# Performance work log

Measured on AMD Instinct MI355X. Metric: run time of the kernel, lower is better.

The kernel has to match this reference:

```python
import jax, jax.numpy as jnp
import numpy as np

N_NODES = 100000
NEG_SLOPE = 0.2  # PyG GATConv default negative_slope


def gat_layer(x, src, dst, W, a_src, a_dst, b):
    """PyG-style GATConv (eval mode: dropout = identity), concat=True.
    x: [N, F_in]; W: [F_in, H*C]; a_src/a_dst: [H, C]; b: [H*C].
    src/dst: [E] edge endpoints (messages flow src -> dst), self-loops included.
    """
    N = x.shape[0]
    H, C = a_src.shape
    h = (x @ W).reshape(N, H, C)                       # [N, H, C]
    al_s = jnp.sum(h * a_src, axis=-1)                 # [N, H]
    al_d = jnp.sum(h * a_dst, axis=-1)                 # [N, H]
    e = jax.nn.leaky_relu(al_s[src] + al_d[dst], NEG_SLOPE)  # [E, H]
    # softmax over incoming edges of each dst node (every node has a self-loop)
    m = jax.ops.segment_max(e, dst, num_segments=N)    # [N, H]
    ex = jnp.exp(e - m[dst])
    s = jax.ops.segment_sum(ex, dst, num_segments=N)   # [N, H]
    alpha = ex / s[dst]                                # [E, H]
    out = jax.ops.segment_sum(h[src] * alpha[:, :, None], dst, num_segments=N)
    return out.reshape(N, H * C) + b


def setup_inputs() -> dict:
    key = jax.random.key(0)
    ks = jax.random.split(key, 12)
    F_in, Hc, H, n_cls = 128, 32, 4, 3
    x = jax.random.normal(ks[0], (N_NODES, F_in), dtype=jnp.float32)
    edge_index = jax.random.randint(ks[1], (2, 1600000), 0, N_NODES, dtype=jnp.int64)
    sc1 = 1.0 / np.sqrt(F_in)
    sc2 = 1.0 / np.sqrt(Hc * H)
    return {
        "x": x,
        "edge_index": edge_index,
        "W1": jax.random.normal(ks[2], (F_in, H * Hc), dtype=jnp.float32) * sc1,
        "a1_src": jax.random.normal(ks[3], (H, Hc), dtype=jnp.float32) * sc1,
        "a1_dst": jax.random.normal(ks[4], (H, Hc), dtype=jnp.float32) * sc1,
        "b1": jnp.zeros((H * Hc,), dtype=jnp.float32),
        "W2": jax.random.normal(ks[5], (H * Hc, Hc), dtype=jnp.float32) * sc2,
        "a2_src": jax.random.normal(ks[6], (1, Hc), dtype=jnp.float32) * sc2,
        "a2_dst": jax.random.normal(ks[7], (1, Hc), dtype=jnp.float32) * sc2,
        "b2": jnp.zeros((Hc,), dtype=jnp.float32),
        "lin_W": jax.random.normal(ks[8], (Hc, n_cls), dtype=jnp.float32) * (1.0 / np.sqrt(Hc)),
        "lin_b": jnp.zeros((n_cls,), dtype=jnp.float32),
    }


def reference(x, edge_index, W1, a1_src, a1_dst, b1, W2, a2_src, a2_dst, b2, lin_W, lin_b):
    N = x.shape[0]
    loops = jnp.arange(N, dtype=edge_index.dtype)
    src = jnp.concatenate([edge_index[0], loops])
    dst = jnp.concatenate([edge_index[1], loops])
    h = jax.nn.elu(gat_layer(x, src, dst, W1, a1_src, a1_dst, b1))
    h = gat_layer(h, src, dst, W2, a2_src, a2_dst, b2)
    pooled = h.mean(axis=0, keepdims=True)             # batch=None path: [1, Hc]
    return jax.nn.softmax(pooled @ lin_W + lin_b, axis=1)
```

## Files before the change

### kernel.cpp

```cpp
#include <hip/hip_runtime.h>
#include <cstdint>
#include <cstddef>

static inline size_t align_up(size_t v, size_t a) { return (v + a - 1) & ~(a - 1); }

#define BCAP 3072

typedef __attribute__((ext_vector_type(8))) short short8;
typedef __attribute__((ext_vector_type(4))) float f32x4;
typedef __attribute__((ext_vector_type(2))) float f32x2;

__device__ inline unsigned short bf16_1(float x) {
  unsigned u = __float_as_uint(x);
  u += 0x7FFFu + ((u >> 16) & 1u);
  return (unsigned short)(u >> 16);
}
__device__ inline unsigned bfpack(float x, float y) {
  unsigned ux = __float_as_uint(x); ux += 0x7FFFu + ((ux >> 16) & 1u);
  unsigned uy = __float_as_uint(y); uy += 0x7FFFu + ((uy >> 16) & 1u);
  return (ux >> 16) | (uy & 0xFFFF0000u);
}

__device__ inline unsigned char fp8_1(float x) {
  return (unsigned char)(__builtin_amdgcn_cvt_pk_fp8_f32(x, x, 0, false) & 0xFF);
}
__device__ inline f32x2 fp8x2_dec(unsigned us) {
  return __builtin_amdgcn_cvt_pk_f32_fp8((int)us, false);
}

__global__ void detect_kernel(const unsigned int* e, int n_check, int* flag) {
  __shared__ int bad;
  if (threadIdx.x == 0) bad = 0;
  __syncthreads();
  for (int i = threadIdx.x; i < n_check; i += blockDim.x)
    if (e[2 * i + 1] != 0u) bad = 1;
  __syncthreads();
  if (threadIdx.x == 0) *flag = bad ? 0 : 1;
}

__device__ inline int load_edge(const void* eidx, int is64, size_t idx) {
  if (is64) return (int)((const long long*)eidx)[idx];
  return ((const int*)eidx)[idx];
}

__global__ void prep_kernel(const float* __restrict__ W1, const float* __restrict__ W2,
                            unsigned short* __restrict__ w1t, unsigned short* __restrict__ w2t) {
  int t = blockIdx.x * 256 + threadIdx.x;
  if (t < 16384) {
    int c = t >> 7, k = t & 127;
    w1t[t] = bf16_1(W1[(size_t)k * 128 + c]);
  } else if (t < 20480) {
    int i = t - 16384;
    int c = i >> 7, k = i & 127;
    w2t[i] = bf16_1(W2[(size_t)k * 32 + c]);
  }
}


__global__ __launch_bounds__(256) void sortA_kernel(const void* eidx, const int* flag, int E,
                                                    int* __restrict__ fillB,
                                                    unsigned* __restrict__ packed, int NB) {
  __shared__ int hist[1024];
  __shared__ int loff[1024];
  __shared__ int lbase[1024];
  __shared__ int lcnt[1024];
  __shared__ unsigned sortedV[2048];
  __shared__ unsigned short sortedB[2048];
  const int t = threadIdx.x;
  const int chunk0 = blockIdx.x * 2048;
  const int cntE = min(2048, E - chunk0);
  const int is64 = *flag;
  int sv[8], dv[8];
  for (int i = t; i < 1024; i += 256) { hist[i] = 0; lcnt[i] = 0; }
  __syncthreads();
#pragma unroll
  for (int it = 0; it < 8; ++it) {
    int li = it * 256 + t;
    if (li < cntE) {
      sv[it] = load_edge(eidx, is64, (size_t)chunk0 + li);
      dv[it] = load_edge(eidx, is64, (size_t)E + chunk0 + li);
      atomicAdd(&hist[dv[it] >> 7], 1);
    }
  }
  __syncthreads();
  for (int b = t; b < NB; b += 256) {
    int h = hist[b];
    if (h) lbase[b] = b * BCAP + atomicAdd(&fillB[b], h);
  }
  {
    int base = t * 4;
    int v[4]; int s = 0;
    __shared__ int sd[256];
#pragma unroll
    for (int j = 0; j < 4; ++j) { v[j] = hist[base + j]; s += v[j]; }
    sd[t] = s; __syncthreads();
    for (int off = 1; off < 256; off <<= 1) {
      int u = (t >= off) ? sd[t - off] : 0;
      __syncthreads();
      sd[t] += u;
      __syncthreads();
    }
    int run = sd[t] - s;
#pragma unroll
    for (int j = 0; j < 4; ++j) { loff[base + j] = run; run += v[j]; }
  }
  __syncthreads();
#pragma unroll
  for (int it = 0; it < 8; ++it) {
    int li = it * 256 + t;
    if (li < cntE) {
      int b = dv[it] >> 7;
      int r = atomicAdd(&lcnt[b], 1);
      int pos = loff[b] + r;
      sortedV[pos] = (unsigned)sv[it] | ((unsigned)(dv[it] & 127) << 20);
      sortedB[pos] = (unsigned short)b;
    }
  }
  __syncthreads();
  for (int li = t; li < cntE; li += 256) {
    int b = sortedB[li];
    packed[(size_t)lbase[b] + (li - loff[b])] = sortedV[li];
  }
}

__global__ __launch_bounds__(256) void buildCSR_kernel(const unsigned* __restrict__ packed,
                                                       const int* __restrict__ fillB,
                                                       int* __restrict__ rowbeg,
                                                       int* __restrict__ rowend,
                                                       int* __restrict__ csr, int N, int NB) {
  __shared__ int cnt[128], ex[128], fill[128];
  const int b = blockIdx.x;
  const int t = threadIdx.x;
  const int beg = b * BCAP;
  const int end = beg + fillB[b];
  const int node0 = b << 7;
  const int nn = min(128, N - node0);
  if (t < 128) { cnt[t] = 0; fill[t] = 0; }
  __syncthreads();
  for (int i = beg + t; i < end; i += 256) {
    int j = (packed[i] >> 20) & 127;
    atomicAdd(&cnt[j], 1);
  }
  __syncthreads();
  if (t < 128) ex[t] = cnt[t];
  __syncthreads();
  for (int off = 1; off < 128; off <<= 1) {
    int u = (t >= off && t < 128) ? ex[t - off] : 0;
    __syncthreads();
    if (t < 128) ex[t] += u;
    __syncthreads();
  }
  if (t < 128) ex[t] -= cnt[t];
  __syncthreads();
  if (t < nn) {
    rowbeg[node0 + t] = beg + ex[t];
    rowend[node0 + t] = beg + ex[t] + cnt[t];
  }
  for (int i = beg + t; i < end; i += 256) {
    unsigned v = packed[i];
    int j = (v >> 20) & 127;
    int r = atomicAdd(&fill[j], 1);
    csr[beg + ex[j] + r] = (int)(v & 0xFFFFFu);
  }
}

__global__ __launch_bounds__(256) void gemm1_mfma(
    const float* __restrict__ x, const unsigned short* __restrict__ w1t,
    const float* __restrict__ a1s, const float* __restrict__ a1d,
    unsigned char* __restrict__ h1f, float* __restrict__ al1s, float* __restrict__ al1d, int N) {
  __shared__ unsigned short sw[128 * 136];
  __shared__ unsigned short sx[64 * 136];
  unsigned char* ftile = (unsigned char*)sx;
  const int t = threadIdx.x;
  const int row0 = blockIdx.x * 64;
  for (int i = t; i < 4096; i += 256) {
    int c = i >> 5, k4 = (i & 31) * 4;
    *(ushort4*)&sw[c * 136 + k4] = *(const ushort4*)&w1t[c * 128 + k4];
  }
  for (int i = t; i < 2048; i += 256) {
    int r = i >> 5, c4 = (i & 31) * 4;
    float4 v = make_float4(0.f, 0.f, 0.f, 0.f);
    if (row0 + r < N) v = *(const float4*)(x + (size_t)(row0 + r) * 128 + c4);
    ushort4 b; b.x = bf16_1(v.x); b.y = bf16_1(v.y); b.z = bf16_1(v.z); b.w = bf16_1(v.w);
    *(ushort4*)&sx[r * 136 + c4] = b;
  }
  __syncthreads();
  const int lane = t & 63, wave = t >> 6;
  const int m = lane & 15, quad = lane >> 4;
  const unsigned short* arow = &sx[(wave * 16 + m) * 136];
  short8 A[4];
#pragma unroll
  for (int ks = 0; ks < 4; ++ks) A[ks] = *(const short8*)&arow[ks * 32 + quad * 8];
  __syncthreads();
  const int lrow = wave * 16 + quad * 4;
#pragma unroll
  for (int nt = 0; nt < 8; ++nt) {
    const unsigned short* brow = &sw[(nt * 16 + m) * 136];
    f32x4 acc = {0.f, 0.f, 0.f, 0.f};
#pragma unroll
    for (int ks = 0; ks < 4; ++ks) {
      short8 B = *(const short8*)&brow[ks * 32 + quad * 8];
      acc = __builtin_amdgcn_mfma_f32_16x16x32_bf16(A[ks], B, acc, 0, 0, 0);
    }
#pragma unroll
    for (int r = 0; r < 4; ++r)
      ftile[(lrow + r) * 128 + nt * 16 + m] = fp8_1(acc[r]);
  }
  __syncthreads();
#pragma unroll
  for (int it = 0; it < 2; ++it) {
    int row = it * 32 + (t >> 3);
    int chunk = t & 7;
    uint4 v = *(const uint4*)&ftile[row * 128 + chunk * 16];
    int grow = row0 + row;
    if (grow < N) *(uint4*)&h1f[(size_t)grow * 128 + chunk * 16] = v;
    unsigned w[4] = {v.x, v.y, v.z, v.w};
    float ps = 0.f, pd = 0.f;
    int cb = chunk * 16;
#pragma unroll
    for (int q = 0; q < 4; ++q) {
      f32x2 lo = __builtin_amdgcn_cvt_pk_f32_fp8((int)w[q], false);
      f32x2 hi = __builtin_amdgcn_cvt_pk_f32_fp8((int)w[q], true);
      int c = cb + q * 4;
      ps += lo[0] * a1s[c] + lo[1] * a1s[c + 1] + hi[0] * a1s[c + 2] + hi[1] * a1s[c + 3];
      pd += lo[0] * a1d[c] + lo[1] * a1d[c + 1] + hi[0] * a1d[c + 2] + hi[1] * a1d[c + 3];
    }
    ps += __shfl_xor(ps, 1); pd += __shfl_xor(pd, 1);
    if ((chunk & 1) == 0 && grow < N) {
      int head = chunk >> 1;
      al1s[(size_t)grow * 4 + head] = ps;
      al1d[(size_t)grow * 4 + head] = pd;
    }
  }
}

__global__ __launch_bounds__(256) void gemm2_mfma(
    const unsigned* __restrict__ houtb, const unsigned short* __restrict__ w2t,
    const float* __restrict__ a2s, const float* __restrict__ a2d,
    unsigned char* __restrict__ h2f, float* __restrict__ al2s, float* __restrict__ al2d, int N) {
  __shared__ unsigned short sw[32 * 136];
  __shared__ unsigned short sx[64 * 136];
  unsigned char* ftile = (unsigned char*)sx;
  const int t = threadIdx.x;
  const int row0 = blockIdx.x * 64;
  for (int i = t; i < 1024; i += 256) {
    int c = i >> 5, k4 = (i & 31) * 4;
    *(ushort4*)&sw[c * 136 + k4] = *(const ushort4*)&w2t[c * 128 + k4];
  }
  for (int i = t; i < 2048; i += 256) {
    int r = i >> 5, d2 = (i & 31) * 2;
    uint2 v = make_uint2(0u, 0u);
    if (row0 + r < N) v = *(const uint2*)(houtb + (size_t)(row0 + r) * 64 + d2);
    *(uint2*)&sx[r * 136 + d2 * 2] = v;
  }
  __syncthreads();
  const int lane = t & 63, wave = t >> 6;
  const int m = lane & 15, quad = lane >> 4;
  const unsigned short* arow = &sx[(wave * 16 + m) * 136];
  short8 A[4];
#pragma unroll
  for (int ks = 0; ks < 4; ++ks) A[ks] = *(const short8*)&arow[ks * 32 + quad * 8];
  __syncthreads();
  const int lrow = wave * 16 + quad * 4;
#pragma unroll
  for (int nt = 0; nt < 2; ++nt) {
    const unsigned short* brow = &sw[(nt * 16 + m) * 136];
    f32x4 acc = {0.f, 0.f, 0.f, 0.f};
#pragma unroll
    for (int ks = 0; ks < 4; ++ks) {
      short8 B = *(const short8*)&brow[ks * 32 + quad * 8];
      acc = __builtin_amdgcn_mfma_f32_16x16x32_bf16(A[ks], B, acc, 0, 0, 0);
    }
#pragma unroll
    for (int r = 0; r < 4; ++r)
      ftile[(lrow + r) * 32 + nt * 16 + m] = fp8_1(acc[r]);
  }
  __syncthreads();
  if (t < 128) {
    int row = t >> 1, chunk = t & 1;
    uint4 v = *(const uint4*)&ftile[row * 32 + chunk * 16];
    int grow = row0 + row;
    if (grow < N) *(uint4*)&h2f[(size_t)grow * 32 + chunk * 16] = v;
    unsigned w[4] = {v.x, v.y, v.z, v.w};
    float ps = 0.f, pd = 0.f;
    int cb = chunk * 16;
#pragma unroll
    for (int q = 0; q < 4; ++q) {
      f32x2 lo = __builtin_amdgcn_cvt_pk_f32_fp8((int)w[q], false);
      f32x2 hi = __builtin_amdgcn_cvt_pk_f32_fp8((int)w[q], true);
      int c = cb + q * 4;
      ps += lo[0] * a2s[c] + lo[1] * a2s[c + 1] + hi[0] * a2s[c + 2] + hi[1] * a2s[c + 3];
      pd += lo[0] * a2d[c] + lo[1] * a2d[c + 1] + hi[0] * a2d[c + 2] + hi[1] * a2d[c + 3];
    }
    ps += __shfl_xor(ps, 1); pd += __shfl_xor(pd, 1);
    if (chunk == 0 && grow < N) { al2s[grow] = ps; al2d[grow] = pd; }
  }
}

__global__ __launch_bounds__(256) void agg1_kernel(
    const int* __restrict__ rowbeg, const int* __restrict__ rowend, const int* __restrict__ csr_src,
    const unsigned* __restrict__ h1w,
    const float* __restrict__ al_s, const float* __restrict__ al_d,
    const float* __restrict__ b1, unsigned* __restrict__ houtb, int N) {
  int t = threadIdx.x;
  int d = (blockIdx.x * 256 + t) >> 6;
  if (d >= N) return;
  int lane = t & 63;
  int half = lane >> 5;
  int l32 = lane & 31;
  int headq = l32 >> 3;
  int combo_e = l32 >> 2;
  int combo_h = l32 & 3;
  float ald_c = al_d[(size_t)d * 4 + combo_h];
  float acc0, acc1, acc2, acc3, den;
  {
    float e = al_s[(size_t)d * 4 + headq] + al_d[(size_t)d * 4 + headq];
    e = fmaxf(e, 0.2f * e);
    float ex = half == 0 ? __expf(e) : 0.f;
    unsigned hv = h1w[(size_t)d * 32 + l32];
    f32x2 lo = __builtin_amdgcn_cvt_pk_f32_fp8((int)hv, false);
    f32x2 hi = __builtin_amdgcn_cvt_pk_f32_fp8((int)hv, true);
    acc0 = ex * lo[0]; acc1 = ex * lo[1]; acc2 = ex * hi[0]; acc3 = ex * hi[1];
    den = ex;
  }
  int beg = rowbeg[d], end = rowend[d];
  for (int i = beg; i < end; i += 8) {
    int idx = i + combo_e;
    int sj = (idx < end) ? csr_src[idx] : d;
    float e = al_s[(size_t)sj * 4 + combo_h] + ald_c;
    e = fmaxf(e, 0.2f * e);
    float ex = __expf(e);
    if (idx >= end) ex = 0.f;
#pragma unroll
    for (int j = 0; j < 4; ++j) {
      int my_e = 2 * j + half;
      int s = __shfl(sj, my_e * 4);
      float exj = __shfl(ex, my_e * 4 + headq);
      unsigned hv = h1w[(size_t)s * 32 + l32];
      f32x2 lo = __builtin_amdgcn_cvt_pk_f32_fp8((int)hv, false);
      f32x2 hi = __builtin_amdgcn_cvt_pk_f32_fp8((int)hv, true);
      acc0 += exj * lo[0]; acc1 += exj * lo[1];
      acc2 += exj * hi[0]; acc3 += exj * hi[1];
      den += exj;
    }
  }
  acc0 += __shfl_xor(acc0, 32);
  acc1 += __shfl_xor(acc1, 32);
  acc2 += __shfl_xor(acc2, 32);
  acc3 += __shfl_xor(acc3, 32);
  den  += __shfl_xor(den, 32);
  float inv = 1.f / den;
  float4 bv = *(const float4*)(b1 + 4 * l32);
  float o0 = acc0 * inv + bv.x;
  float o1 = acc1 * inv + bv.y;
  float o2 = acc2 * inv + bv.z;
  float o3 = acc3 * inv + bv.w;
  o0 = o0 > 0.f ? o0 : expm1f(o0);
  o1 = o1 > 0.f ? o1 : expm1f(o1);
  o2 = o2 > 0.f ? o2 : expm1f(o2);
  o3 = o3 > 0.f ? o3 : expm1f(o3);
  if (half == 0) {
    uint2 u; u.x = bfpack(o0, o1); u.y = bfpack(o2, o3);
    *(uint2*)&houtb[(size_t)d * 64 + 2 * l32] = u;
  }
}

__global__ __launch_bounds__(256) void agg2_kernel(
    const int* __restrict__ rowbeg, const int* __restrict__ rowend, const int* __restrict__ csr_src,
    const unsigned short* __restrict__ h2q,
    const float* __restrict__ al_s, const float* __restrict__ al_d,
    float* __restrict__ partial, int N) {
  __shared__ float sp[16 * 32];
  int t = threadIdx.x;
  int lane = t & 63;
  int l16 = t & 15;
  int slot = t >> 4;
  int node = (blockIdx.x * 256 + t) >> 4;
  float ox = 0.f, oy = 0.f;
  if (node < N) {
    float ald = al_d[node];
    float accx, accy, den;
    {
      float e = al_s[node] + ald;
      e = fmaxf(e, 0.2f * e);
      float ex = __expf(e);
      f32x2 h = fp8x2_dec(h2q[(size_t)node * 16 + l16]);
      accx = ex * h[0]; accy = ex * h[1]; den = ex;
    }
    int beg = rowbeg[node], end = rowend[node];
    for (int i = beg; i < end; i += 8) {
      int idx = i + (l16 & 7);
      int sj = (idx < end) ? csr_src[idx] : node;
      float e = al_s[sj] + ald;
      e = fmaxf(e, 0.2f * e);
      float ex = __expf(e);
      if (idx >= end) ex = 0.f;
#pragma unroll
      for (int j = 0; j < 8; ++j) {
        int lsrc = (lane & 48) | j;
        int s = __shfl(sj, lsrc);
        float exj = __shfl(ex, lsrc);
        f32x2 h = fp8x2_dec(h2q[(size_t)s * 16 + l16]);
        accx += exj * h[0];
        accy += exj * h[1];
        den += exj;
      }
    }
    float inv = 1.f / den;
    ox = accx * inv; oy = accy * inv;
  }
  sp[slot * 32 + 2 * l16] = ox;
  sp[slot * 32 + 2 * l16 + 1] = oy;
  __syncthreads();
  if (t < 32) {
    float s = 0.f;
#pragma unroll
    for (int j = 0; j < 16; ++j) s += sp[j * 32 + t];
    partial[(size_t)blockIdx.x * 32 + t] = s;
  }
}

__global__ __launch_bounds__(256) void reduce_kernel(
    const float* __restrict__ partial, int nb, float* __restrict__ partial2) {
  __shared__ float sp[8 * 32];
  int t = threadIdx.x;
  int slot = t >> 5, c = t & 31;
  int row0 = blockIdx.x * 8 + slot;
  float s = 0.f;
  for (int i = row0; i < nb; i += 1024) s += partial[(size_t)i * 32 + c];
  sp[slot * 32 + c] = s;
  __syncthreads();
  if (t < 32) {
    float tot = 0.f;
#pragma unroll
    for (int j = 0; j < 8; ++j) tot += sp[j * 32 + t];
    partial2[(size_t)blockIdx.x * 32 + t] = tot;
  }
}

__global__ void final_kernel(const float* __restrict__ partial2, int nb,
                             const float* __restrict__ b2, const float* __restrict__ linW,
                             const float* __restrict__ linb, float* __restrict__ out, int N) {
  __shared__ float sd[256];
  __shared__ float pooled[32];
  int t = threadIdx.x;
  int c = t & 31, g = t >> 5;
  float s = 0.f;
  for (int i = g; i < nb; i += 8) s += partial2[(size_t)i * 32 + c];
  sd[t] = s; __syncthreads();
  if (t < 32) {
    float tot = 0.f;
#pragma unroll
    for (int j = 0; j < 8; ++j) tot += sd[j * 32 + t];
    pooled[t] = tot / (float)N + b2[t];
  }
  __syncthreads();
  if (t == 0) {
    float lg[3];
    for (int j = 0; j < 3; ++j) lg[j] = linb[j];
    for (int cc = 0; cc < 32; ++cc)
      for (int j = 0; j < 3; ++j) lg[j] += pooled[cc] * linW[cc * 3 + j];
    float m = fmaxf(lg[0], fmaxf(lg[1], lg[2]));
    float e0 = __expf(lg[0] - m), e1 = __expf(lg[1] - m), e2 = __expf(lg[2] - m);
    float inv = 1.f / (e0 + e1 + e2);
    out[0] = e0 * inv; out[1] = e1 * inv; out[2] = e2 * inv;
  }
}

extern "C" void kernel_launch(void* const* d_in, const int* in_sizes, int n_in,
                              void* d_out, int out_size, void* d_ws, size_t ws_size,
                              hipStream_t stream) {
  const float* x    = (const float*)d_in[0];
  const void*  eidx = d_in[1];
  const float* W1   = (const float*)d_in[2];
  const float* a1s  = (const float*)d_in[3];
  const float* a1d  = (const float*)d_in[4];
  const float* b1   = (const float*)d_in[5];
  const float* W2   = (const float*)d_in[6];
  const float* a2s  = (const float*)d_in[7];
  const float* a2d  = (const float*)d_in[8];
  const float* b2   = (const float*)d_in[9];
  const float* linW = (const float*)d_in[10];
  const float* linb = (const float*)d_in[11];
  float* out = (float*)d_out;

  const int N = in_sizes[0] / 128;
  const int E = in_sizes[1] / 2;
  const int NB = (N + 127) >> 7;

  char* ws = (char*)d_ws;
  size_t off = 0;
  auto alloc = [&](size_t bytes) -> void* {
    size_t o = off;
    off = align_up(off + bytes, 256);
    return (void*)(ws + o);
  };
  int* fillB  = (int*)alloc((size_t)1024 * sizeof(int));
  int* flag   = (int*)alloc(sizeof(int));
  int* rowbeg = (int*)alloc((size_t)N * sizeof(int));
  int* rowend = (int*)alloc((size_t)N * sizeof(int));
  unsigned* packed = (unsigned*)alloc((size_t)NB * BCAP * sizeof(unsigned));
  int* csr    = (int*)alloc((size_t)NB * BCAP * sizeof(int));
  float* al1s = (float*)alloc((size_t)N * 4 * sizeof(float));
  float* al1d = (float*)alloc((size_t)N * 4 * sizeof(float));
  float* al2s = (float*)alloc((size_t)N * sizeof(float));
  float* al2d = (float*)alloc((size_t)N * sizeof(float));
  unsigned short* w1t = (unsigned short*)alloc(16384 * sizeof(unsigned short));
  unsigned short* w2t = (unsigned short*)alloc(4096 * sizeof(unsigned short));
  unsigned char* h1f  = (unsigned char*)alloc((size_t)N * 128);
  unsigned* houtb = (unsigned*)alloc((size_t)N * 64 * sizeof(unsigned));
  unsigned char* h2f  = (unsigned char*)alloc((size_t)N * 32);
  const int nAggBlocks = (N + 15) / 16;
  float* partial  = (float*)alloc((size_t)nAggBlocks * 32 * sizeof(float));
  float* partial2 = (float*)alloc((size_t)128 * 32 * sizeof(float));

  hipMemsetAsync(fillB, 0, (size_t)1024 * sizeof(int), stream);
  int ncheck = E < 512 ? E : 512;
  detect_kernel<<<1, 256, 0, stream>>>((const unsigned int*)eidx, ncheck, flag);
  prep_kernel<<<80, 256, 0, stream>>>(W1, W2, w1t, w2t);

  sortA_kernel<<<(E + 2047) / 2048, 256, 0, stream>>>(eidx, flag, E, fillB, packed, NB);
  buildCSR_kernel<<<NB, 256, 0, stream>>>(packed, fillB, rowbeg, rowend, csr, N, NB);

  const int gemmBlocks = (N + 63) / 64;
  gemm1_mfma<<<gemmBlocks, 256, 0, stream>>>(x, w1t, a1s, a1d, h1f, al1s, al1d, N);
  agg1_kernel<<<(N * 64 + 255) / 256, 256, 0, stream>>>(
      rowbeg, rowend, csr, (const unsigned*)h1f, al1s, al1d, b1, houtb, N);
  gemm2_mfma<<<gemmBlocks, 256, 0, stream>>>(houtb, w2t, a2s, a2d, h2f, al2s, al2d, N);
  agg2_kernel<<<(N * 16 + 255) / 256, 256, 0, stream>>>(
      rowbeg, rowend, csr, (const unsigned short*)h2f, al2s, al2d, partial, N);
  reduce_kernel<<<128, 256, 0, stream>>>(partial, nAggBlocks, partial2);
  final_kernel<<<1, 256, 0, stream>>>(partial2, 128, b2, linW, linb, out, N);
}
```

Measured before the change: 283.4 us.

## Restructure GAT aggregation kernels to process multiple edges per lane group with wider loads

Both aggregation kernels are reorganized so that each lane handles 8 fp8 channels via a uint2 load, and several edge groups are processed in parallel within a wave. Each lane computes its own attention exponent, which removes the per-edge shuffle broadcasts, and partial sums are combined with an xor-shuffle reduction at the end. The layer-1 ELU now uses the fast exp minus one instead of expm1f. The aim is more memory-level parallelism in the gathers and fewer shuffle instructions, at the cost of more registers and redundant exp evaluations.

New measurement: 285.7 us. No clear change (+0.8%).

```diff
diff --git a/kernel.cpp b/kernel.cpp
--- a/kernel.cpp
+++ b/kernel.cpp
@@ -23,9 +23,6 @@
 
 __device__ inline unsigned char fp8_1(float x) {
   return (unsigned char)(__builtin_amdgcn_cvt_pk_fp8_f32(x, x, 0, false) & 0xFF);
-}
-__device__ inline f32x2 fp8x2_dec(unsigned us) {
-  return __builtin_amdgcn_cvt_pk_f32_fp8((int)us, false);
 }
 
 __global__ void detect_kernel(const unsigned int* e, int n_check, int* flag) {
@@ -297,120 +294,165 @@
   }
 }
 
+#define DEC8(HV, EX)                                                        \
+  {                                                                         \
+    f32x2 _l0 = __builtin_amdgcn_cvt_pk_f32_fp8((int)(HV).x, false);        \
+    f32x2 _h0 = __builtin_amdgcn_cvt_pk_f32_fp8((int)(HV).x, true);         \
+    f32x2 _l1 = __builtin_amdgcn_cvt_pk_f32_fp8((int)(HV).y, false);        \
+    f32x2 _h1 = __builtin_amdgcn_cvt_pk_f32_fp8((int)(HV).y, true);         \
+    acc0 += (EX) * _l0[0]; acc1 += (EX) * _l0[1];                           \
+    acc2 += (EX) * _h0[0]; acc3 += (EX) * _h0[1];                           \
+    acc4 += (EX) * _l1[0]; acc5 += (EX) * _l1[1];                           \
+    acc6 += (EX) * _h1[0]; acc7 += (EX) * _h1[1];                           \
+    den += (EX);                                                            \
+  }
+
 __global__ __launch_bounds__(256) void agg1_kernel(
     const int* __restrict__ rowbeg, const int* __restrict__ rowend, const int* __restrict__ csr_src,
-    const unsigned* __restrict__ h1w,
+    const unsigned char* __restrict__ h1f,
     const float* __restrict__ al_s, const float* __restrict__ al_d,
     const float* __restrict__ b1, unsigned* __restrict__ houtb, int N) {
   int t = threadIdx.x;
   int d = (blockIdx.x * 256 + t) >> 6;
   if (d >= N) return;
   int lane = t & 63;
-  int half = lane >> 5;
-  int l32 = lane & 31;
-  int headq = l32 >> 3;
-  int combo_e = l32 >> 2;
-  int combo_h = l32 & 3;
-  float ald_c = al_d[(size_t)d * 4 + combo_h];
-  float acc0, acc1, acc2, acc3, den;
+  int e_id = lane >> 4;
+  int c8 = lane & 15;
+  int head = c8 >> 2;
+  const float ald = al_d[d * 4 + head];
+  float acc0 = 0.f, acc1 = 0.f, acc2 = 0.f, acc3 = 0.f;
+  float acc4 = 0.f, acc5 = 0.f, acc6 = 0.f, acc7 = 0.f, den = 0.f;
   {
-    float e = al_s[(size_t)d * 4 + headq] + al_d[(size_t)d * 4 + headq];
+    float e = al_s[d * 4 + head] + ald;
     e = fmaxf(e, 0.2f * e);
-    float ex = half == 0 ? __expf(e) : 0.f;
-    unsigned hv = h1w[(size_t)d * 32 + l32];
-    f32x2 lo = __builtin_amdgcn_cvt_pk_f32_fp8((int)hv, false);
-    f32x2 hi = __builtin_amdgcn_cvt_pk_f32_fp8((int)hv, true);
-    acc0 = ex * lo[0]; acc1 = ex * lo[1]; acc2 = ex * hi[0]; acc3 = ex * hi[1];
-    den = ex;
-  }
-  int beg = rowbeg[d], end = rowend[d];
+    float ex = (e_id == 0) ? __expf(e) : 0.f;
+    uint2 hv = *(const uint2*)(h1f + d * 128 + c8 * 8);
+    DEC8(hv, ex);
+  }
+  const int beg = rowbeg[d], end = rowend[d];
   for (int i = beg; i < end; i += 8) {
-    int idx = i + combo_e;
-    int sj = (idx < end) ? csr_src[idx] : d;
-    float e = al_s[(size_t)sj * 4 + combo_h] + ald_c;
-    e = fmaxf(e, 0.2f * e);
-    float ex = __expf(e);
-    if (idx >= end) ex = 0.f;
-#pragma unroll
-    for (int j = 0; j < 4; ++j) {
-      int my_e = 2 * j + half;
-      int s = __shfl(sj, my_e * 4);
-      float exj = __shfl(ex, my_e * 4 + headq);
-      unsigned hv = h1w[(size_t)s * 32 + l32];
-      f32x2 lo = __builtin_amdgcn_cvt_pk_f32_fp8((int)hv, false);
-      f32x2 hi = __builtin_amdgcn_cvt_pk_f32_fp8((int)hv, true);
-      acc0 += exj * lo[0]; acc1 += exj * lo[1];
-      acc2 += exj * hi[0]; acc3 += exj * hi[1];
-      den += exj;
-    }
-  }
-  acc0 += __shfl_xor(acc0, 32);
-  acc1 += __shfl_xor(acc1, 32);
-  acc2 += __shfl_xor(acc2, 32);
-  acc3 += __shfl_xor(acc3, 32);
+    int idx0 = i + e_id;
+    int idx1 = idx0 + 4;
+    int sj0 = (idx0 < end) ? csr_src[idx0] : d;
+    int sj1 = (idx1 < end) ? csr_src[idx1] : d;
+    float as0 = al_s[sj0 * 4 + head];
+    float as1 = al_s[sj1 * 4 + head];
+    uint2 hv0 = *(const uint2*)(h1f + sj0 * 128 + c8 * 8);
+    uint2 hv1 = *(const uint2*)(h1f + sj1 * 128 + c8 * 8);
+    float e0 = as0 + ald;
+    e0 = fmaxf(e0, 0.2f * e0);
+    float ex0 = __expf(e0);
+    if (idx0 >= end) ex0 = 0.f;
+    float e1 = as1 + ald;
+    e1 = fmaxf(e1, 0.2f * e1);
+    float ex1 = __expf(e1);
+    if (idx1 >= end) ex1 = 0.f;
+    DEC8(hv0, ex0);
+    DEC8(hv1, ex1);
+  }
+  acc0 += __shfl_xor(acc0, 16); acc1 += __shfl_xor(acc1, 16);
+  acc2 += __shfl_xor(acc2, 16); acc3 += __shfl_xor(acc3, 16);
+  acc4 += __shfl_xor(acc4, 16); acc5 += __shfl_xor(acc5, 16);
+  acc6 += __shfl_xor(acc6, 16); acc7 += __shfl_xor(acc7, 16);
+  den  += __shfl_xor(den, 16);
+  acc0 += __shfl_xor(acc0, 32); acc1 += __shfl_xor(acc1, 32);
+  acc2 += __shfl_xor(acc2, 32); acc3 += __shfl_xor(acc3, 32);
+  acc4 += __shfl_xor(acc4, 32); acc5 += __shfl_xor(acc5, 32);
+  acc6 += __shfl_xor(acc6, 32); acc7 += __shfl_xor(acc7, 32);
   den  += __shfl_xor(den, 32);
   float inv = 1.f / den;
-  float4 bv = *(const float4*)(b1 + 4 * l32);
-  float o0 = acc0 * inv + bv.x;
-  float o1 = acc1 * inv + bv.y;
-  float o2 = acc2 * inv + bv.z;
-  float o3 = acc3 * inv + bv.w;
-  o0 = o0 > 0.f ? o0 : expm1f(o0);
-  o1 = o1 > 0.f ? o1 : expm1f(o1);
-  o2 = o2 > 0.f ? o2 : expm1f(o2);
-  o3 = o3 > 0.f ? o3 : expm1f(o3);
-  if (half == 0) {
-    uint2 u; u.x = bfpack(o0, o1); u.y = bfpack(o2, o3);
-    *(uint2*)&houtb[(size_t)d * 64 + 2 * l32] = u;
+  float4 bv0 = *(const float4*)(b1 + 8 * c8);
+  float4 bv1 = *(const float4*)(b1 + 8 * c8 + 4);
+  float o0 = acc0 * inv + bv0.x;
+  float o1 = acc1 * inv + bv0.y;
+  float o2 = acc2 * inv + bv0.z;
+  float o3 = acc3 * inv + bv0.w;
+  float o4 = acc4 * inv + bv1.x;
+  float o5 = acc5 * inv + bv1.y;
+  float o6 = acc6 * inv + bv1.z;
+  float o7 = acc7 * inv + bv1.w;
+  o0 = o0 > 0.f ? o0 : __expf(o0) - 1.f;
+  o1 = o1 > 0.f ? o1 : __expf(o1) - 1.f;
+  o2 = o2 > 0.f ? o2 : __expf(o2) - 1.f;
+  o3 = o3 > 0.f ? o3 : __expf(o3) - 1.f;
+  o4 = o4 > 0.f ? o4 : __expf(o4) - 1.f;
+  o5 = o5 > 0.f ? o5 : __expf(o5) - 1.f;
+  o6 = o6 > 0.f ? o6 : __expf(o6) - 1.f;
+  o7 = o7 > 0.f ? o7 : __expf(o7) - 1.f;
+  if (e_id == 0) {
+    uint4 u;
+    u.x = bfpack(o0, o1); u.y = bfpack(o2, o3);
+    u.z = bfpack(o4, o5); u.w = bfpack(o6, o7);
+    *(uint4*)&houtb[d * 64 + 4 * c8] = u;
   }
 }
 
 __global__ __launch_bounds__(256) void agg2_kernel(
     const int* __restrict__ rowbeg, const int* __restrict__ rowend, const int* __restrict__ csr_src,
-    const unsigned short* __restrict__ h2q,
+    const unsigned char* __restrict__ h2f,
     const float* __restrict__ al_s, const float* __restrict__ al_d,
     float* __restrict__ partial, int N) {
   __shared__ float sp[16 * 32];
   int t = threadIdx.x;
-  int lane = t & 63;
   int l16 = t & 15;
   int slot = t >> 4;
   int node = (blockIdx.x * 256 + t) >> 4;
-  float ox = 0.f, oy = 0.f;
+  int e_id = l16 >> 2;
+  int c8 = l16 & 3;
+  float o0 = 0.f, o1 = 0.f, o2 = 0.f, o3 = 0.f;
+  float o4 = 0.f, o5 = 0.f, o6 = 0.f, o7 = 0.f;
   if (node < N) {
-    float ald = al_d[node];
-    float accx, accy, den;
+    const float ald = al_d[node];
+    float acc0 = 0.f, acc1 = 0.f, acc2 = 0.f, acc3 = 0.f;
+    float acc4 = 0.f, acc5 = 0.f, acc6 = 0.f, acc7 = 0.f, den = 0.f;
     {
       float e = al_s[node] + ald;
       e = fmaxf(e, 0.2f * e);
-      float ex = __expf(e);
-      f32x2 h = fp8x2_dec(h2q[(size_t)node * 16 + l16]);
-      accx = ex * h[0]; accy = ex * h[1]; den = ex;
-    }
-    int beg = rowbeg[node], end = rowend[node];
+      float ex = (e_id == 0) ? __expf(e) : 0.f;
+      uint2 hv = *(const uint2*)(h2f + node * 32 + c8 * 8);
+      DEC8(hv, ex);
+    }
+    const int beg = rowbeg[node], end = rowend[node];
     for (int i = beg; i < end; i += 8) {
-      int idx = i + (l16 & 7);
-      int sj = (idx < end) ? csr_src[idx] : node;
-      float e = al_s[sj] + ald;
-      e = fmaxf(e, 0.2f * e);
-      float ex = __expf(e);
-      if (idx >= end) ex = 0.f;
-#pragma unroll
-      for (int j = 0; j < 8; ++j) {
-        int lsrc = (lane & 48) | j;
-        int s = __shfl(sj, lsrc);
-        float exj = __shfl(ex, lsrc);
-        f32x2 h = fp8x2_dec(h2q[(size_t)s * 16 + l16]);
-        accx += exj * h[0];
-        accy += exj * h[1];
-        den += exj;
-      }
-    }
+      int idx0 = i + e_id;
+      int idx1 = idx0 + 4;
+      int sj0 = (idx0 < end) ? csr_src[idx0] : node;
+      int sj1 = (idx1 < end) ? csr_src[idx1] : node;
+      float as0 = al_s[sj0];
+      float as1 = al_s[sj1];
+      uint2 hv0 = *(const uint2*)(h2f + sj0 * 32 + c8 * 8);
+      uint2 hv1 = *(const uint2*)(h2f + sj1 * 32 + c8 * 8);
+      float e0 = as0 + ald;
+      e0 = fmaxf(e0, 0.2f * e0);
+      float ex0 = __expf(e0);
+      if (idx0 >= end) ex0 = 0.f;
+      float e1 = as1 + ald;
+      e1 = fmaxf(e1, 0.2f * e1);
+      float ex1 = __expf(e1);
+      if (idx1 >= end) ex1 = 0.f;
+      DEC8(hv0, ex0);
+      DEC8(hv1, ex1);
+    }
+    acc0 += __shfl_xor(acc0, 4); acc1 += __shfl_xor(acc1, 4);
+    acc2 += __shfl_xor(acc2, 4); acc3 += __shfl_xor(acc3, 4);
+    acc4 += __shfl_xor(acc4, 4); acc5 += __shfl_xor(acc5, 4);
+    acc6 += __shfl_xor(acc6, 4); acc7 += __shfl_xor(acc7, 4);
+    den  += __shfl_xor(den, 4);
+    acc0 += __shfl_xor(acc0, 8); acc1 += __shfl_xor(acc1, 8);
+    acc2 += __shfl_xor(acc2, 8); acc3 += __shfl_xor(acc3, 8);
+    acc4 += __shfl_xor(acc4, 8); acc5 += __shfl_xor(acc5, 8);
+    acc6 += __shfl_xor(acc6, 8); acc7 += __shfl_xor(acc7, 8);
+    den  += __shfl_xor(den, 8);
     float inv = 1.f / den;
-    ox = accx * inv; oy = accy * inv;
-  }
-  sp[slot * 32 + 2 * l16] = ox;
-  sp[slot * 32 + 2 * l16 + 1] = oy;
+    o0 = acc0 * inv; o1 = acc1 * inv; o2 = acc2 * inv; o3 = acc3 * inv;
+    o4 = acc4 * inv; o5 = acc5 * inv; o6 = acc6 * inv; o7 = acc7 * inv;
+  }
+  if (e_id == 0) {
+    float4 v0 = {o0, o1, o2, o3};
+    float4 v1 = {o4, o5, o6, o7};
+    *(float4*)&sp[slot * 32 + 8 * c8] = v0;
+    *(float4*)&sp[slot * 32 + 8 * c8 + 4] = v1;
+  }
   __syncthreads();
   if (t < 32) {
     float s = 0.f;
@@ -525,10 +567,10 @@
   const int gemmBlocks = (N + 63) / 64;
   gemm1_mfma<<<gemmBlocks, 256, 0, stream>>>(x, w1t, a1s, a1d, h1f, al1s, al1d, N);
   agg1_kernel<<<(N * 64 + 255) / 256, 256, 0, stream>>>(
-      rowbeg, rowend, csr, (const unsigned*)h1f, al1s, al1d, b1, houtb, N);
+      rowbeg, rowend, csr, h1f, al1s, al1d, b1, houtb, N);
   gemm2_mfma<<<gemmBlocks, 256, 0, stream>>>(houtb, w2t, a2s, a2d, h2f, al2s, al2d, N);
   agg2_kernel<<<(N * 16 + 255) / 256, 256, 0, stream>>>(
-      rowbeg, rowend, csr, (const unsigned short*)h2f, al2s, al2d, partial, N);
+      rowbeg, rowend, csr, h2f, al2s, al2d, partial, N);
   reduce_kernel<<<128, 256, 0, stream>>>(partial, nAggBlocks, partial2);
   final_kernel<<<1, 256, 0, stream>>>(partial2, 128, b2, linW, linb, out, N);
 }
```
